# Kernel optimization log

Measured on AMD Instinct MI355X. Metric: run time of the kernel, lower is better.

## Reference

```python
import jax, jax.numpy as jnp
import numpy as np

N = 50000        # vertices
E = 1_600_000    # edges (avg degree 32)
CIN = 8          # in_channels (scalar input features)
COUT = 32        # out_channels (tangent vector channels, complex -> trailing dim 2)
R = 2            # n_corr_rings (radial profile rings)
EPS = 1e-6


def setup_inputs() -> dict:
    key = jax.random.key(0)
    ks = jax.random.split(key, 12)
    x = jax.random.normal(ks[0], (N, CIN), jnp.float32)
    edge_index = jax.random.randint(ks[1], (2, E), 0, N, dtype=jnp.int32)
    # precomputed per-edge transport * radial interpolation coefficients (re, im) per ring
    pcmp_gather = jax.random.normal(ks[2], (E, R, 2), jnp.float32)
    # TransField learned radial profile and phase offset (offset=True)
    W_rad = jax.random.normal(ks[3], (R, CIN, COUT), jnp.float32) / np.float32(np.sqrt(R * CIN))
    phase = jax.random.normal(ks[4], (COUT,), jnp.float32)
    # TangentNonLin bias after the field conv
    b_nl = jax.random.normal(ks[5], (COUT,), jnp.float32) * 0.1
    # three TangentPerceptrons: complex-linear (real weight shared over re/im) + TangentNonLin
    sc = np.float32(1.0 / np.sqrt(COUT))
    W1 = jax.random.normal(ks[6], (COUT, COUT), jnp.float32) * sc
    b1 = jax.random.normal(ks[7], (COUT,), jnp.float32) * 0.1
    W2 = jax.random.normal(ks[8], (COUT, COUT), jnp.float32) * sc
    b2 = jax.random.normal(ks[9], (COUT,), jnp.float32) * 0.1
    W3 = jax.random.normal(ks[10], (COUT, COUT), jnp.float32) * sc
    b3 = jax.random.normal(ks[11], (COUT,), jnp.float32) * 0.1
    return dict(x=x, edge_index=edge_index, pcmp_gather=pcmp_gather, W_rad=W_rad,
                phase=phase, b_nl=b_nl, W1=W1, b1=b1, W2=W2, b2=b2, W3=W3, b3=b3)


def tangent_nonlin(z, b):
    # ReLU on magnitude with learned per-channel bias, phase preserved
    mag = jnp.sqrt(jnp.sum(z * z, axis=-1) + EPS)           # [N, C]
    scale = jax.nn.relu(mag + b) / mag                      # [N, C]
    return z * scale[..., None]


def trans_field(x, src, dst, pcmp_gather, W_rad, phase, n_nodes):
    xs = x[src]                                             # gather: [E, CIN]
    t = jnp.einsum('ei,rio->ero', xs, W_rad)                # [E, R, COUT]
    # modulate by complex transport coeffs per ring, sum rings -> [E, COUT, 2]
    msg = jnp.sum(t[..., None] * pcmp_gather[:, :, None, :], axis=1)
    agg = jax.ops.segment_sum(msg, dst, num_segments=n_nodes)  # scatter: [N, COUT, 2]
    # learned phase offset: rotate each output channel by e^{i*phase}
    c, s = jnp.cos(phase), jnp.sin(phase)
    re = agg[..., 0] * c - agg[..., 1] * s
    im = agg[..., 0] * s + agg[..., 1] * c
    return jnp.stack([re, im], axis=-1)                     # [N, COUT, 2]


def reference(x, edge_index, pcmp_gather, W_rad, phase, b_nl, W1, b1, W2, b2, W3, b3):
    src, dst = edge_index[0], edge_index[1]
    y = trans_field(x, src, dst, pcmp_gather, W_rad, phase, x.shape[0])
    y = tangent_nonlin(y, b_nl)
    for W, b in ((W1, b1), (W2, b2), (W3, b3)):
        y = jnp.einsum('nik,io->nok', y, W)                 # complex-linear (shared real weight)
        y = tangent_nonlin(y, b)
    return y
```

## Files before the change

### kernel.cpp

```cpp
#include <hip/hip_runtime.h>

#define CIN 8
#define COUT 32
#define NR 2
#define EPSF 1e-6f

#define BSH 5
#define BNODES 32
#define NBMAX 2048
#define CHUNK 4096
#define BINT 512
#define BREG (CHUNK / BINT)
#define IDBITS 21
#define IDMASK ((1u << IDBITS) - 1u)
#define SRCMASK 0x03FFFFFFu
#define PSTAGE 1792
#define AREG (PSTAGE / 256)

__global__ __launch_bounds__(256) void bucket_hist(
    const int* __restrict__ eidx, int* __restrict__ bucketCnt, int E, int nb)
{
    __shared__ int cnt[NBMAX];
    for (int i = threadIdx.x; i < nb; i += 256) cnt[i] = 0;
    __syncthreads();
    for (int e = blockIdx.x * 256 + threadIdx.x; e < E; e += gridDim.x * 256)
        atomicAdd(&cnt[eidx[E + e] >> BSH], 1);
    __syncthreads();
    for (int i = threadIdx.x; i < nb; i += 256)
        if (cnt[i]) atomicAdd(&bucketCnt[i], cnt[i]);
}

__global__ __launch_bounds__(1024) void scan_init(
    const int* __restrict__ bucketCnt, int* __restrict__ bucketBase,
    int* __restrict__ gCursor, int nb)
{
    __shared__ int sA[NBMAX], sB[NBMAX];
    for (int i = threadIdx.x; i < NBMAX; i += 1024)
        sA[i] = (i < nb) ? bucketCnt[i] : 0;
    __syncthreads();
    int* src = sA; int* dst = sB;
    for (int off = 1; off < NBMAX; off <<= 1) {
        for (int i = threadIdx.x; i < NBMAX; i += 1024)
            dst[i] = src[i] + (i >= off ? src[i - off] : 0);
        __syncthreads();
        int* tmp = src; src = dst; dst = tmp;
    }
    for (int i = threadIdx.x; i < nb; i += 1024) {
        int incl = src[i];
        int base = incl - bucketCnt[i];
        bucketBase[i] = base;
        gCursor[i] = base;
        if (i == nb - 1) bucketBase[nb] = incl;
    }
}

template<bool PACKED>
__global__ __launch_bounds__(BINT) void binify(
    const int* __restrict__ eidx, int* __restrict__ gCursor,
    unsigned* __restrict__ outMeta,
    float4*   __restrict__ pcmpS,
    const float* __restrict__ pcmp, int E, int nb)
{
    __shared__ int cnt[NBMAX];
    __shared__ int sIncl[NBMAX];
    __shared__ int gbase[NBMAX];
    __shared__ int wsum[8];
    __shared__ unsigned sid[CHUNK];
    __shared__ unsigned short bucketOf[CHUNK];

    const int e0 = blockIdx.x * CHUNK;
    const int num = min(CHUNK, E - e0);
    const int t = threadIdx.x;
    const int lane = t & 63, wid = t >> 6;

    for (int i = t; i < nb; i += BINT) cnt[i] = 0;
    __syncthreads();

    int dreg[BREG];
#pragma unroll
    for (int kk = 0; kk < BREG; ++kk) {
        int k = t + kk * BINT;
        if (k < num) {
            dreg[kk] = eidx[E + e0 + k];
            atomicAdd(&cnt[dreg[kk] >> BSH], 1);
        }
    }
    __syncthreads();

    {
        int j0 = t * 4;
        int v0 = (j0 + 0 < nb) ? cnt[j0 + 0] : 0;
        int v1 = (j0 + 1 < nb) ? cnt[j0 + 1] : 0;
        int v2 = (j0 + 2 < nb) ? cnt[j0 + 2] : 0;
        int v3 = (j0 + 3 < nb) ? cnt[j0 + 3] : 0;
        int p0 = v0, p1 = p0 + v1, p2 = p1 + v2, p3 = p2 + v3;
        int incl = p3;
#pragma unroll
        for (int off = 1; off < 64; off <<= 1) {
            int u = __shfl_up(incl, off, 64);
            if (lane >= off) incl += u;
        }
        int laneEx = incl - p3;
        if (lane == 63) wsum[wid] = incl;
        __syncthreads();
        if (t == 0) {
            int acc = 0;
#pragma unroll
            for (int i = 0; i < 8; ++i) { int w = wsum[i]; wsum[i] = acc; acc += w; }
        }
        __syncthreads();
        int off0 = wsum[wid] + laneEx;
        sIncl[j0 + 0] = off0 + p0;
        sIncl[j0 + 1] = off0 + p1;
        sIncl[j0 + 2] = off0 + p2;
        sIncl[j0 + 3] = off0 + p3;
    }
    __syncthreads();

    for (int b = t; b < nb; b += BINT) {
        int c = sIncl[b] - (b ? sIncl[b - 1] : 0);
        gbase[b] = c ? atomicAdd(&gCursor[b], c) : 0;
    }
    __syncthreads();
    for (int i = t; i < nb; i += BINT) cnt[i] = 0;
    __syncthreads();

#pragma unroll
    for (int kk = 0; kk < BREG; ++kk) {
        int k = t + kk * BINT;
        if (k < num) {
            int e = e0 + k;
            int d = dreg[kk];
            int b = d >> BSH;
            int slot = (b ? sIncl[b - 1] : 0) + atomicAdd(&cnt[b], 1);
            sid[slot] = ((unsigned)(d & (BNODES - 1)) << IDBITS) | (unsigned)e;
            bucketOf[slot] = (unsigned short)b;
        }
    }
    __syncthreads();

    for (int s = t; s < num; s += BINT) {
        int b = bucketOf[s];
        int intra = s - (b ? sIncl[b - 1] : 0);
        unsigned v = sid[s];
        int pos = gbase[b] + intra;
        if (PACKED) {
            int id = v & IDMASK;
            unsigned dl = v >> IDBITS;
            unsigned sv = (unsigned)eidx[id];
            outMeta[pos] = (dl << 26) | sv;
            pcmpS[pos] = *reinterpret_cast<const float4*>(pcmp + (size_t)id * 4);
        } else {
            outMeta[pos] = v;
        }
    }
}

template<bool SRC16>
__global__ __launch_bounds__(256, 6) void fused_team_kernel(
    const float* __restrict__ x,
    const float4* __restrict__ pcmpS,
    const unsigned* __restrict__ meta,
    const int* __restrict__ bucketBase,
    const float* __restrict__ W_rad, const float* __restrict__ phase,
    const float* __restrict__ b_nl,
    const float* __restrict__ W1, const float* __restrict__ b1,
    const float* __restrict__ W2, const float* __restrict__ b2,
    const float* __restrict__ W3, const float* __restrict__ b3,
    float* __restrict__ out, int N)
{
    __shared__ float sWrad[NR * CIN][COUT];
    __shared__ float sPh[COUT][2];
    __shared__ float sBias[4][COUT];
    __shared__ unsigned srtPk[PSTAGE];
    __shared__ unsigned short srtK[SRC16 ? 2 : PSTAGE];
    __shared__ float Qbuf[BNODES][33];
    __shared__ int cnt[BNODES], segS[BNODES], padL[BNODES], cur[BNODES];

    for (int i = threadIdx.x; i < NR * CIN * COUT; i += 256) ((float*)sWrad)[i] = W_rad[i];
    if (threadIdx.x < COUT) {
        float sn, cs; __sincosf(phase[threadIdx.x], &sn, &cs);
        sPh[threadIdx.x][0] = cs; sPh[threadIdx.x][1] = sn;
        sBias[0][threadIdx.x] = b_nl[threadIdx.x];
        sBias[1][threadIdx.x] = b1[threadIdx.x];
        sBias[2][threadIdx.x] = b2[threadIdx.x];
        sBias[3][threadIdx.x] = b3[threadIdx.x];
    }
    if (threadIdx.x < BNODES) cnt[threadIdx.x] = 0;

    const int start = bucketBase[blockIdx.x];
    const int total = bucketBase[blockIdx.x + 1] - start;
    const bool fb = (total > PSTAGE);
    __syncthreads();

    unsigned mreg[AREG];
    const int staged = fb ? 0 : total;
#pragma unroll
    for (int kk = 0; kk < AREG; ++kk) {
        int k = threadIdx.x + (kk << 8);
        if (k < staged) {
            mreg[kk] = meta[start + k];
            atomicAdd(&cnt[mreg[kk] >> 26], 1);
        }
    }
    __syncthreads();

    if (threadIdx.x < BNODES) {
        int v = cnt[threadIdx.x];
        int m = v;
        m = max(m, __shfl_xor(m, 1, 32));
        m = max(m, __shfl_xor(m, 2, 32));
        m = max(m, __shfl_xor(m, 4, 32));
        int incl = v;
#pragma unroll
        for (int off = 1; off < BNODES; off <<= 1) {
            int u = __shfl_up(incl, off, 32);
            if ((int)threadIdx.x >= off) incl += u;
        }
        segS[threadIdx.x] = incl - v;
        cur[threadIdx.x]  = incl - v;
        padL[threadIdx.x] = m;
    }
    __syncthreads();

    if (!fb) {
#pragma unroll
        for (int kk = 0; kk < AREG; ++kk) {
            int k = threadIdx.x + (kk << 8);
            if (k < staged) {
                unsigned m = mreg[kk];
                int pos = atomicAdd(&cur[m >> 26], 1);
                if (SRC16) {
                    srtPk[pos] = ((unsigned)k << 16) | (m & 0xFFFFu);
                } else {
                    srtPk[pos] = m & SRCMASK;
                    srtK[pos] = (unsigned short)k;
                }
            }
        }
    }
    __syncthreads();

    const int c    = threadIdx.x & 31;
    const int sub  = threadIdx.x >> 5;
    const int team = c >> 3;
    const int il   = c & 7;
    const int gl   = sub * 4 + team;
    const int node0 = blockIdx.x << BSH;

    float4 qa = {0.f, 0.f, 0.f, 0.f};
    if (!fb) {
        const int base  = segS[gl];
        const int myCnt = cnt[gl];
        const int Tw    = padL[gl];
        const int last  = total - 1;
#pragma unroll 4
        for (int t = 0; t < Tw; ++t) {
            bool act = (t < myCnt);
            int slot = min(base + t, last);
            int sv, kk2;
            if (SRC16) {
                unsigned p = srtPk[slot];
                sv = (int)(p & 0xFFFFu); kk2 = (int)(p >> 16);
            } else {
                sv = (int)srtPk[slot]; kk2 = (int)srtK[slot];
            }
            float4 pc4 = pcmpS[start + kk2];
            float xf = act ? x[(sv << 3) + il] : 0.f;
            qa.x += xf * pc4.x;
            qa.y += xf * pc4.y;
            qa.z += xf * pc4.z;
            qa.w += xf * pc4.w;
        }
    } else {
        const float4* pcG = pcmpS + start;
        for (int t = 0; t < total; ++t) {
            unsigned m = meta[start + t];
            if ((int)(m >> 26) == gl) {
                float4 pc4 = pcG[t];
                float xf = x[(size_t)(m & SRCMASK) * CIN + il];
                qa.x += xf * pc4.x;
                qa.y += xf * pc4.y;
                qa.z += xf * pc4.z;
                qa.w += xf * pc4.w;
            }
        }
    }

    Qbuf[gl][2 * il]      = qa.x;
    Qbuf[gl][2 * il + 1]  = qa.y;
    Qbuf[gl][16 + 2 * il] = qa.z;
    Qbuf[gl][17 + 2 * il] = qa.w;

#pragma unroll
    for (int r = 0; r < 4; ++r) {
        const int gln = sub * 4 + r;
        const int n   = node0 + gln;
        float a0 = 0.f, a1 = 0.f;
#pragma unroll
        for (int ri = 0; ri < NR * CIN; ++ri) {
            float w = sWrad[ri][c];
            a0 += w * Qbuf[gln][2 * ri];
            a1 += w * Qbuf[gln][2 * ri + 1];
        }
        float cs = sPh[c][0], sn = sPh[c][1];
        float re = a0 * cs - a1 * sn;
        float im = a0 * sn + a1 * cs;
        float mag = sqrtf(re * re + im * im + EPSF);
        float sc  = fmaxf(mag + sBias[0][c], 0.f) / mag;
        re *= sc; im *= sc;
#pragma unroll
        for (int L = 0; L < 3; ++L) {
            const float* __restrict__ Wl = (L == 0) ? W1 : (L == 1) ? W2 : W3;
            float bb0 = 0.f, bb1 = 0.f;
#pragma unroll
            for (int i = 0; i < COUT; ++i) {
                float w = Wl[i * COUT + c];
                bb0 += w * __shfl(re, i, 32);
                bb1 += w * __shfl(im, i, 32);
            }
            float m2 = sqrtf(bb0 * bb0 + bb1 * bb1 + EPSF);
            float s2 = fmaxf(m2 + sBias[L + 1][c], 0.f) / m2;
            re = bb0 * s2; im = bb1 * s2;
        }
        if (n < N) {
            float2 v; v.x = re; v.y = im;
            *reinterpret_cast<float2*>(out + ((n << 6) + (c << 1))) = v;
        }
    }
}

__global__ __launch_bounds__(256) void fused_bucket_fallback(
    const float* __restrict__ x, const int* __restrict__ eidx,
    const float* __restrict__ pcmp, const int* __restrict__ bucketBase,
    const unsigned* __restrict__ sorted,
    const float* __restrict__ W_rad, const float* __restrict__ phase,
    const float* __restrict__ b_nl,
    const float* __restrict__ W1, const float* __restrict__ b1,
    const float* __restrict__ W2, const float* __restrict__ b2,
    const float* __restrict__ W3, const float* __restrict__ b3,
    float* __restrict__ out, int N)
{
    __shared__ float Q[BNODES][COUT];
    __shared__ float sWrad[NR * CIN][COUT];
    __shared__ float sW[3][COUT][COUT];
    __shared__ float sPh[COUT][2];
    __shared__ float sBias[4][COUT];

    for (int i = threadIdx.x; i < BNODES * COUT; i += 256) ((float*)Q)[i] = 0.f;
    for (int i = threadIdx.x; i < NR * CIN * COUT; i += 256) ((float*)sWrad)[i] = W_rad[i];
    for (int i = threadIdx.x; i < COUT * COUT; i += 256) {
        ((float*)sW[0])[i] = W1[i];
        ((float*)sW[1])[i] = W2[i];
        ((float*)sW[2])[i] = W3[i];
    }
    if (threadIdx.x < COUT) {
        float sn, cs; __sincosf(phase[threadIdx.x], &sn, &cs);
        sPh[threadIdx.x][0] = cs; sPh[threadIdx.x][1] = sn;
        sBias[0][threadIdx.x] = b_nl[threadIdx.x];
        sBias[1][threadIdx.x] = b1[threadIdx.x];
        sBias[2][threadIdx.x] = b2[threadIdx.x];
        sBias[3][threadIdx.x] = b3[threadIdx.x];
    }
    __syncthreads();

    const int c   = threadIdx.x & 31;
    const int sub = threadIdx.x >> 5;
    const int i_idx  = (c >> 1) & 7;
    const int pc_off = ((c >> 4) << 1) | (c & 1);
    const int start = bucketBase[blockIdx.x];
    const int end   = bucketBase[blockIdx.x + 1];

    for (int p = start + sub; p < end; p += 8) {
        unsigned v0 = sorted[p];
        int id0 = v0 & IDMASK;
        int s0 = eidx[id0];
        atomicAdd(&Q[v0 >> IDBITS][c],
                  x[(size_t)s0 * CIN + i_idx] * pcmp[(size_t)id0 * 4 + pc_off]);
    }
    __syncthreads();

    const int node0 = blockIdx.x << BSH;
#pragma unroll
    for (int r = 0; r < 4; ++r) {
        const int gl = r * 8 + sub;
        const int n  = node0 + gl;
        float a0 = 0.f, a1 = 0.f;
#pragma unroll
        for (int ri = 0; ri < NR * CIN; ++ri) {
            float w = sWrad[ri][c];
            a0 += w * Q[gl][2 * ri];
            a1 += w * Q[gl][2 * ri + 1];
        }
        float cs = sPh[c][0], sn = sPh[c][1];
        float re = a0 * cs - a1 * sn;
        float im = a0 * sn + a1 * cs;
        float mag = sqrtf(re * re + im * im + EPSF);
        float sc  = fmaxf(mag + sBias[0][c], 0.f) / mag;
        re *= sc; im *= sc;
#pragma unroll
        for (int L = 0; L < 3; ++L) {
            float b0 = 0.f, b1v = 0.f;
#pragma unroll
            for (int i = 0; i < COUT; ++i) {
                float w = sW[L][i][c];
                b0  += w * __shfl(re, i, 32);
                b1v += w * __shfl(im, i, 32);
            }
            float m2 = sqrtf(b0 * b0 + b1v * b1v + EPSF);
            float s2 = fmaxf(m2 + sBias[L + 1][c], 0.f) / m2;
            re = b0 * s2; im = b1v * s2;
        }
        if (n < N) {
            float2 v; v.x = re; v.y = im;
            *reinterpret_cast<float2*>(out + ((size_t)n * COUT + c) * 2) = v;
        }
    }
}

extern "C" void kernel_launch(void* const* d_in, const int* in_sizes, int n_in,
                              void* d_out, int out_size, void* d_ws, size_t ws_size,
                              hipStream_t stream)
{
    const float* x     = (const float*)d_in[0];
    const int*   eidx  = (const int*)  d_in[1];
    const float* pcmp  = (const float*)d_in[2];
    const float* W_rad = (const float*)d_in[3];
    const float* phase = (const float*)d_in[4];
    const float* b_nl  = (const float*)d_in[5];
    const float* W1    = (const float*)d_in[6];
    const float* b1    = (const float*)d_in[7];
    const float* W2    = (const float*)d_in[8];
    const float* b2    = (const float*)d_in[9];
    const float* W3    = (const float*)d_in[10];
    const float* b3    = (const float*)d_in[11];
    float* out = (float*)d_out;

    const int N = in_sizes[0] / CIN;
    const int E = in_sizes[1] / 2;
    const int nb = (N + BNODES - 1) >> BSH;
    const int nchunk = (E + CHUNK - 1) / CHUNK;

    float4*   pcmpS      = (float4*)d_ws;
    unsigned* meta       = (unsigned*)(pcmpS + E);
    int*      bucketCnt  = (int*)(meta + E);
    int*      bucketBase = bucketCnt + NBMAX;
    int*      gCursor    = bucketBase + NBMAX + 1;
    size_t needed = (size_t)((char*)(gCursor + NBMAX) - (char*)d_ws);

    if (ws_size >= needed) {
        hipMemsetAsync(bucketCnt, 0, (size_t)nb * sizeof(int), stream);
        bucket_hist<<<256, 256, 0, stream>>>(eidx, bucketCnt, E, nb);
        scan_init<<<1, 1024, 0, stream>>>(bucketCnt, bucketBase, gCursor, nb);
        binify<true><<<nchunk, BINT, 0, stream>>>(eidx, gCursor, meta, pcmpS, pcmp, E, nb);
        if (N <= 65536) {
            fused_team_kernel<true><<<nb, 256, 0, stream>>>(
                x, pcmpS, meta, bucketBase,
                W_rad, phase, b_nl, W1, b1, W2, b2, W3, b3, out, N);
        } else {
            fused_team_kernel<false><<<nb, 256, 0, stream>>>(
                x, pcmpS, meta, bucketBase,
                W_rad, phase, b_nl, W1, b1, W2, b2, W3, b3, out, N);
        }
    } else {
        int*      bc = (int*)d_ws;
        int*      bb = bc + NBMAX;
        int*      gc = bb + NBMAX + 1;
        unsigned* so = (unsigned*)(gc + NBMAX);
        hipMemsetAsync(bc, 0, (size_t)nb * sizeof(int), stream);
        bucket_hist<<<256, 256, 0, stream>>>(eidx, bc, E, nb);
        scan_init<<<1, 1024, 0, stream>>>(bc, bb, gc, nb);
        binify<false><<<nchunk, BINT, 0, stream>>>(eidx, gc, so, nullptr, pcmp, E, nb);
        fused_bucket_fallback<<<nb, 256, 0, stream>>>(
            x, eidx, pcmp, bb, so,
            W_rad, phase, b_nl, W1, b1, W2, b2, W3, b3, out, N);
    }
}
```

Measured before the change: 165.9 us.

## Split per-node edge sort into separate reorder kernel and build CSR layout

Adds a reorder kernel that sorts each bucket's edges by destination node in shared memory and writes pcmp coefficients and source ids back in node-contiguous (CSR) order, together with per-node start offsets. The fused kernel then walks each node's edge range directly with 4-way unrolled, coalesced loads, dropping the in-kernel histogram, scan, atomic scatter and padded max-length loop, and its launch bounds are raised for occupancy. The cost is an extra kernel launch and an extra read/write pass over the pcmp and source arrays. gCursor is reused as the big-bucket flag array.

```diff
diff --git a/kernel.cpp b/kernel.cpp
--- a/kernel.cpp
+++ b/kernel.cpp
@@ -15,7 +15,6 @@
 #define IDMASK ((1u << IDBITS) - 1u)
 #define SRCMASK 0x03FFFFFFu
 #define PSTAGE 1792
-#define AREG (PSTAGE / 256)
 
 __global__ __launch_bounds__(256) void bucket_hist(
     const int* __restrict__ eidx, int* __restrict__ bucketCnt, int E, int nb)
@@ -32,7 +31,7 @@
 
 __global__ __launch_bounds__(1024) void scan_init(
     const int* __restrict__ bucketCnt, int* __restrict__ bucketBase,
-    int* __restrict__ gCursor, int nb)
+    int* __restrict__ gCursor, int* __restrict__ nodeStart, int N, int nb)
 {
     __shared__ int sA[NBMAX], sB[NBMAX];
     for (int i = threadIdx.x; i < NBMAX; i += 1024)
@@ -50,7 +49,10 @@
         int base = incl - bucketCnt[i];
         bucketBase[i] = base;
         gCursor[i] = base;
-        if (i == nb - 1) bucketBase[nb] = incl;
+        if (i == nb - 1) {
+            bucketBase[nb] = incl;
+            if (nodeStart) nodeStart[N] = incl;
+        }
     }
 }
 
@@ -156,12 +158,71 @@
     }
 }
 
-template<bool SRC16>
-__global__ __launch_bounds__(256, 6) void fused_team_kernel(
+__global__ __launch_bounds__(256) void reorder(
+    const unsigned* __restrict__ meta,
+    float4* __restrict__ pcmpS,
+    unsigned* __restrict__ srcN,
+    const int* __restrict__ bucketBase,
+    int* __restrict__ nodeStart,
+    int* __restrict__ bigFlag,
+    int N)
+{
+    __shared__ float4 pcL[PSTAGE];
+    __shared__ unsigned srcL[PSTAGE];
+    __shared__ int cnt[BNODES], cur[BNODES];
+
+    const int bkt = blockIdx.x;
+    const int start = bucketBase[bkt];
+    const int total = bucketBase[bkt + 1] - start;
+    const int node0 = bkt << BSH;
+
+    if (threadIdx.x < BNODES) cnt[threadIdx.x] = 0;
+    __syncthreads();
+
+    for (int k = threadIdx.x; k < total; k += 256)
+        atomicAdd(&cnt[meta[start + k] >> 26], 1);
+    __syncthreads();
+
+    if (threadIdx.x < BNODES) {
+        int v = cnt[threadIdx.x];
+        int incl = v;
+#pragma unroll
+        for (int off = 1; off < BNODES; off <<= 1) {
+            int u = __shfl_up(incl, off, 32);
+            if ((int)threadIdx.x >= off) incl += u;
+        }
+        int ex = incl - v;
+        cur[threadIdx.x] = ex;
+        int n = node0 + threadIdx.x;
+        if (n < N) nodeStart[n] = start + ex;
+    }
+    if (threadIdx.x == 0) bigFlag[bkt] = (total > PSTAGE) ? 1 : 0;
+    __syncthreads();
+
+    if (total > PSTAGE) return;
+
+    for (int k = threadIdx.x; k < total; k += 256) {
+        unsigned m = meta[start + k];
+        int pos = atomicAdd(&cur[m >> 26], 1);
+        pcL[pos] = pcmpS[start + k];
+        srcL[pos] = m & SRCMASK;
+    }
+    __syncthreads();
+
+    for (int j = threadIdx.x; j < total; j += 256) {
+        pcmpS[start + j] = pcL[j];
+        srcN[start + j] = srcL[j];
+    }
+}
+
+__global__ __launch_bounds__(256, 8) void fused_csr(
     const float* __restrict__ x,
     const float4* __restrict__ pcmpS,
+    const unsigned* __restrict__ srcN,
     const unsigned* __restrict__ meta,
     const int* __restrict__ bucketBase,
+    const int* __restrict__ bigFlag,
+    const int* __restrict__ nodeStart,
     const float* __restrict__ W_rad, const float* __restrict__ phase,
     const float* __restrict__ b_nl,
     const float* __restrict__ W1, const float* __restrict__ b1,
@@ -172,10 +233,7 @@
     __shared__ float sWrad[NR * CIN][COUT];
     __shared__ float sPh[COUT][2];
     __shared__ float sBias[4][COUT];
-    __shared__ unsigned srtPk[PSTAGE];
-    __shared__ unsigned short srtK[SRC16 ? 2 : PSTAGE];
     __shared__ float Qbuf[BNODES][33];
-    __shared__ int cnt[BNODES], segS[BNODES], padL[BNODES], cur[BNODES];
 
     for (int i = threadIdx.x; i < NR * CIN * COUT; i += 256) ((float*)sWrad)[i] = W_rad[i];
     if (threadIdx.x < COUT) {
@@ -186,59 +244,6 @@
         sBias[2][threadIdx.x] = b2[threadIdx.x];
         sBias[3][threadIdx.x] = b3[threadIdx.x];
     }
-    if (threadIdx.x < BNODES) cnt[threadIdx.x] = 0;
-
-    const int start = bucketBase[blockIdx.x];
-    const int total = bucketBase[blockIdx.x + 1] - start;
-    const bool fb = (total > PSTAGE);
-    __syncthreads();
-
-    unsigned mreg[AREG];
-    const int staged = fb ? 0 : total;
-#pragma unroll
-    for (int kk = 0; kk < AREG; ++kk) {
-        int k = threadIdx.x + (kk << 8);
-        if (k < staged) {
-            mreg[kk] = meta[start + k];
-            atomicAdd(&cnt[mreg[kk] >> 26], 1);
-        }
-    }
-    __syncthreads();
-
-    if (threadIdx.x < BNODES) {
-        int v = cnt[threadIdx.x];
-        int m = v;
-        m = max(m, __shfl_xor(m, 1, 32));
-        m = max(m, __shfl_xor(m, 2, 32));
-        m = max(m, __shfl_xor(m, 4, 32));
-        int incl = v;
-#pragma unroll
-        for (int off = 1; off < BNODES; off <<= 1) {
-            int u = __shfl_up(incl, off, 32);
-            if ((int)threadIdx.x >= off) incl += u;
-        }
-        segS[threadIdx.x] = incl - v;
-        cur[threadIdx.x]  = incl - v;
-        padL[threadIdx.x] = m;
-    }
-    __syncthreads();
-
-    if (!fb) {
-#pragma unroll
-        for (int kk = 0; kk < AREG; ++kk) {
-            int k = threadIdx.x + (kk << 8);
-            if (k < staged) {
-                unsigned m = mreg[kk];
-                int pos = atomicAdd(&cur[m >> 26], 1);
-                if (SRC16) {
-                    srtPk[pos] = ((unsigned)k << 16) | (m & 0xFFFFu);
-                } else {
-                    srtPk[pos] = m & SRCMASK;
-                    srtK[pos] = (unsigned short)k;
-                }
-            }
-        }
-    }
     __syncthreads();
 
     const int c    = threadIdx.x & 31;
@@ -247,37 +252,47 @@
     const int il   = c & 7;
     const int gl   = sub * 4 + team;
     const int node0 = blockIdx.x << BSH;
+    const int n = node0 + gl;
 
     float4 qa = {0.f, 0.f, 0.f, 0.f};
-    if (!fb) {
-        const int base  = segS[gl];
-        const int myCnt = cnt[gl];
-        const int Tw    = padL[gl];
-        const int last  = total - 1;
-#pragma unroll 4
-        for (int t = 0; t < Tw; ++t) {
-            bool act = (t < myCnt);
-            int slot = min(base + t, last);
-            int sv, kk2;
-            if (SRC16) {
-                unsigned p = srtPk[slot];
-                sv = (int)(p & 0xFFFFu); kk2 = (int)(p >> 16);
-            } else {
-                sv = (int)srtPk[slot]; kk2 = (int)srtK[slot];
+    const bool big = (bigFlag[blockIdx.x] != 0);
+    if (!big) {
+        if (n < N) {
+            int p  = nodeStart[n];
+            int pe = nodeStart[n + 1];
+#pragma unroll 2
+            for (; p + 4 <= pe; p += 4) {
+                unsigned s0 = srcN[p],     s1 = srcN[p + 1];
+                unsigned s2 = srcN[p + 2], s3 = srcN[p + 3];
+                float4 a = pcmpS[p],     b = pcmpS[p + 1];
+                float4 cc = pcmpS[p + 2], d = pcmpS[p + 3];
+                float x0 = x[(s0 << 3) + il];
+                float x1 = x[(s1 << 3) + il];
+                float x2 = x[(s2 << 3) + il];
+                float x3 = x[(s3 << 3) + il];
+                qa.x += x0 * a.x;  qa.y += x0 * a.y;  qa.z += x0 * a.z;  qa.w += x0 * a.w;
+                qa.x += x1 * b.x;  qa.y += x1 * b.y;  qa.z += x1 * b.z;  qa.w += x1 * b.w;
+                qa.x += x2 * cc.x; qa.y += x2 * cc.y; qa.z += x2 * cc.z; qa.w += x2 * cc.w;
+                qa.x += x3 * d.x;  qa.y += x3 * d.y;  qa.z += x3 * d.z;  qa.w += x3 * d.w;
             }
-            float4 pc4 = pcmpS[start + kk2];
-            float xf = act ? x[(sv << 3) + il] : 0.f;
-            qa.x += xf * pc4.x;
-            qa.y += xf * pc4.y;
-            qa.z += xf * pc4.z;
-            qa.w += xf * pc4.w;
+            for (; p < pe; ++p) {
+                unsigned sv = srcN[p];
+                float4 pc4 = pcmpS[p];
+                float xf = x[(sv << 3) + il];
+                qa.x += xf * pc4.x;
+                qa.y += xf * pc4.y;
+                qa.z += xf * pc4.z;
+                qa.w += xf * pc4.w;
+            }
         }
     } else {
+        const int start = bucketBase[blockIdx.x];
+        const int total = bucketBase[blockIdx.x + 1] - start;
         const float4* pcG = pcmpS + start;
-        for (int t = 0; t < total; ++t) {
-            unsigned m = meta[start + t];
+        for (int t2 = 0; t2 < total; ++t2) {
+            unsigned m = meta[start + t2];
             if ((int)(m >> 26) == gl) {
-                float4 pc4 = pcG[t];
+                float4 pc4 = pcG[t2];
                 float xf = x[(size_t)(m & SRCMASK) * CIN + il];
                 qa.x += xf * pc4.x;
                 qa.y += xf * pc4.y;
@@ -295,7 +310,7 @@
 #pragma unroll
     for (int r = 0; r < 4; ++r) {
         const int gln = sub * 4 + r;
-        const int n   = node0 + gln;
+        const int no  = node0 + gln;
         float a0 = 0.f, a1 = 0.f;
 #pragma unroll
         for (int ri = 0; ri < NR * CIN; ++ri) {
@@ -323,9 +338,9 @@
             float s2 = fmaxf(m2 + sBias[L + 1][c], 0.f) / m2;
             re = bb0 * s2; im = bb1 * s2;
         }
-        if (n < N) {
+        if (no < N) {
             float2 v; v.x = re; v.y = im;
-            *reinterpret_cast<float2*>(out + ((n << 6) + (c << 1))) = v;
+            *reinterpret_cast<float2*>(out + ((no << 6) + (c << 1))) = v;
         }
     }
 }
@@ -443,7 +458,9 @@
 
     float4*   pcmpS      = (float4*)d_ws;
     unsigned* meta       = (unsigned*)(pcmpS + E);
-    int*      bucketCnt  = (int*)(meta + E);
+    unsigned* srcN       = meta + E;
+    int*      nodeStart  = (int*)(srcN + E);
+    int*      bucketCnt  = nodeStart + N + 1;
     int*      bucketBase = bucketCnt + NBMAX;
     int*      gCursor    = bucketBase + NBMAX + 1;
     size_t needed = (size_t)((char*)(gCursor + NBMAX) - (char*)d_ws);
@@ -451,17 +468,14 @@
     if (ws_size >= needed) {
         hipMemsetAsync(bucketCnt, 0, (size_t)nb * sizeof(int), stream);
         bucket_hist<<<256, 256, 0, stream>>>(eidx, bucketCnt, E, nb);
-        scan_init<<<1, 1024, 0, stream>>>(bucketCnt, bucketBase, gCursor, nb);
+        scan_init<<<1, 1024, 0, stream>>>(bucketCnt, bucketBase, gCursor,
+                                          nodeStart, N, nb);
         binify<true><<<nchunk, BINT, 0, stream>>>(eidx, gCursor, meta, pcmpS, pcmp, E, nb);
-        if (N <= 65536) {
-            fused_team_kernel<true><<<nb, 256, 0, stream>>>(
-                x, pcmpS, meta, bucketBase,
-                W_rad, phase, b_nl, W1, b1, W2, b2, W3, b3, out, N);
-        } else {
-            fused_team_kernel<false><<<nb, 256, 0, stream>>>(
-                x, pcmpS, meta, bucketBase,
-                W_rad, phase, b_nl, W1, b1, W2, b2, W3, b3, out, N);
-        }
+        reorder<<<nb, 256, 0, stream>>>(meta, pcmpS, srcN, bucketBase,
+                                        nodeStart, gCursor, N);
+        fused_csr<<<nb, 256, 0, stream>>>(
+            x, pcmpS, srcN, meta, bucketBase, gCursor, nodeStart,
+            W_rad, phase, b_nl, W1, b1, W2, b2, W3, b3, out, N);
     } else {
         int*      bc = (int*)d_ws;
         int*      bb = bc + NBMAX;
@@ -469,7 +483,7 @@
         unsigned* so = (unsigned*)(gc + NBMAX);
         hipMemsetAsync(bc, 0, (size_t)nb * sizeof(int), stream);
         bucket_hist<<<256, 256, 0, stream>>>(eidx, bc, E, nb);
-        scan_init<<<1, 1024, 0, stream>>>(bc, bb, gc, nb);
+        scan_init<<<1, 1024, 0, stream>>>(bc, bb, gc, nullptr, N, nb);
         binify<false><<<nchunk, BINT, 0, stream>>>(eidx, gc, so, nullptr, pcmp, E, nb);
         fused_bucket_fallback<<<nb, 256, 0, stream>>>(
             x, eidx, pcmp, bb, so,
```

Result: slower. 186.9 us (+12.7%).

## Double block threads in fused kernel, splitting edge gather across two halves

Applied to the files above, without the earlier changes.

The fused per-bucket kernel now launches 512 threads instead of 256. Two halves of the block each process alternate edges of every node's segment and write separate partial sums into a doubled Qbuf, which are added before the dense perceptron stage. Each sub-warp then finishes two nodes instead of four. This aims to shorten the serial per-node gather loop and raise memory-level parallelism. The cost is an extra barrier, extra shared memory, and a tighter register budget from the launch bound of 512 threads with minimum 8 blocks.

```diff
diff --git a/kernel.cpp b/kernel.cpp
--- a/kernel.cpp
+++ b/kernel.cpp
@@ -15,7 +15,8 @@
 #define IDMASK ((1u << IDBITS) - 1u)
 #define SRCMASK 0x03FFFFFFu
 #define PSTAGE 1792
-#define AREG (PSTAGE / 256)
+#define FTH 512
+#define AR2 ((PSTAGE + FTH - 1) / FTH)
 
 __global__ __launch_bounds__(256) void bucket_hist(
     const int* __restrict__ eidx, int* __restrict__ bucketCnt, int E, int nb)
@@ -157,7 +158,7 @@
 }
 
 template<bool SRC16>
-__global__ __launch_bounds__(256, 6) void fused_team_kernel(
+__global__ __launch_bounds__(FTH, 8) void fused_team_kernel(
     const float* __restrict__ x,
     const float4* __restrict__ pcmpS,
     const unsigned* __restrict__ meta,
@@ -174,10 +175,10 @@
     __shared__ float sBias[4][COUT];
     __shared__ unsigned srtPk[PSTAGE];
     __shared__ unsigned short srtK[SRC16 ? 2 : PSTAGE];
-    __shared__ float Qbuf[BNODES][33];
+    __shared__ float Qbuf[2][BNODES][33];
     __shared__ int cnt[BNODES], segS[BNODES], padL[BNODES], cur[BNODES];
 
-    for (int i = threadIdx.x; i < NR * CIN * COUT; i += 256) ((float*)sWrad)[i] = W_rad[i];
+    for (int i = threadIdx.x; i < NR * CIN * COUT; i += FTH) ((float*)sWrad)[i] = W_rad[i];
     if (threadIdx.x < COUT) {
         float sn, cs; __sincosf(phase[threadIdx.x], &sn, &cs);
         sPh[threadIdx.x][0] = cs; sPh[threadIdx.x][1] = sn;
@@ -193,11 +194,11 @@
     const bool fb = (total > PSTAGE);
     __syncthreads();
 
-    unsigned mreg[AREG];
+    unsigned mreg[AR2];
     const int staged = fb ? 0 : total;
 #pragma unroll
-    for (int kk = 0; kk < AREG; ++kk) {
-        int k = threadIdx.x + (kk << 8);
+    for (int kk = 0; kk < AR2; ++kk) {
+        int k = threadIdx.x + kk * FTH;
         if (k < staged) {
             mreg[kk] = meta[start + k];
             atomicAdd(&cnt[mreg[kk] >> 26], 1);
@@ -225,8 +226,8 @@
 
     if (!fb) {
 #pragma unroll
-        for (int kk = 0; kk < AREG; ++kk) {
-            int k = threadIdx.x + (kk << 8);
+        for (int kk = 0; kk < AR2; ++kk) {
+            int k = threadIdx.x + kk * FTH;
             if (k < staged) {
                 unsigned m = mreg[kk];
                 int pos = atomicAdd(&cur[m >> 26], 1);
@@ -243,9 +244,10 @@
 
     const int c    = threadIdx.x & 31;
     const int sub  = threadIdx.x >> 5;
-    const int team = c >> 3;
+    const int team4 = c >> 3;
     const int il   = c & 7;
-    const int gl   = sub * 4 + team;
+    const int gl   = (sub & 7) * 4 + team4;
+    const int half = sub >> 3;
     const int node0 = blockIdx.x << BSH;
 
     float4 qa = {0.f, 0.f, 0.f, 0.f};
@@ -255,7 +257,7 @@
         const int Tw    = padL[gl];
         const int last  = total - 1;
 #pragma unroll 4
-        for (int t = 0; t < Tw; ++t) {
+        for (int t = half; t < Tw; t += 2) {
             bool act = (t < myCnt);
             int slot = min(base + t, last);
             int sv, kk2;
@@ -274,7 +276,7 @@
         }
     } else {
         const float4* pcG = pcmpS + start;
-        for (int t = 0; t < total; ++t) {
+        for (int t = half; t < total; t += 2) {
             unsigned m = meta[start + t];
             if ((int)(m >> 26) == gl) {
                 float4 pc4 = pcG[t];
@@ -287,21 +289,22 @@
         }
     }
 
-    Qbuf[gl][2 * il]      = qa.x;
-    Qbuf[gl][2 * il + 1]  = qa.y;
-    Qbuf[gl][16 + 2 * il] = qa.z;
-    Qbuf[gl][17 + 2 * il] = qa.w;
-
-#pragma unroll
-    for (int r = 0; r < 4; ++r) {
-        const int gln = sub * 4 + r;
+    Qbuf[half][gl][2 * il]      = qa.x;
+    Qbuf[half][gl][2 * il + 1]  = qa.y;
+    Qbuf[half][gl][16 + 2 * il] = qa.z;
+    Qbuf[half][gl][17 + 2 * il] = qa.w;
+    __syncthreads();
+
+#pragma unroll
+    for (int r = 0; r < 2; ++r) {
+        const int gln = sub * 2 + r;
         const int n   = node0 + gln;
         float a0 = 0.f, a1 = 0.f;
 #pragma unroll
         for (int ri = 0; ri < NR * CIN; ++ri) {
             float w = sWrad[ri][c];
-            a0 += w * Qbuf[gln][2 * ri];
-            a1 += w * Qbuf[gln][2 * ri + 1];
+            a0 += w * (Qbuf[0][gln][2 * ri]     + Qbuf[1][gln][2 * ri]);
+            a1 += w * (Qbuf[0][gln][2 * ri + 1] + Qbuf[1][gln][2 * ri + 1]);
         }
         float cs = sPh[c][0], sn = sPh[c][1];
         float re = a0 * cs - a1 * sn;
@@ -454,11 +457,11 @@
         scan_init<<<1, 1024, 0, stream>>>(bucketCnt, bucketBase, gCursor, nb);
         binify<true><<<nchunk, BINT, 0, stream>>>(eidx, gCursor, meta, pcmpS, pcmp, E, nb);
         if (N <= 65536) {
-            fused_team_kernel<true><<<nb, 256, 0, stream>>>(
+            fused_team_kernel<true><<<nb, FTH, 0, stream>>>(
                 x, pcmpS, meta, bucketBase,
                 W_rad, phase, b_nl, W1, b1, W2, b2, W3, b3, out, N);
         } else {
-            fused_team_kernel<false><<<nb, 256, 0, stream>>>(
+            fused_team_kernel<false><<<nb, FTH, 0, stream>>>(
                 x, pcmpS, meta, bucketBase,
                 W_rad, phase, b_nl, W1, b1, W2, b2, W3, b3, out, N);
         }
```

Result: slower. 173.4 us (+4.6%).
